# Kernel tuning notes

Hardware: AMD Instinct MI355X
Metric: run time of the kernel (lower is better)

The kernel has to match this reference:

```python
import jax, jax.numpy as jnp
import numpy as np

L_PAIRS = 2
K_NEG = 64
TEMP = 0.1
EPS = 1e-8  # torch F.cosine_similarity default eps


def _cos(a, b):
    # cosine similarity along last axis, torch-style eps clamping of norms
    na = jnp.maximum(jnp.linalg.norm(a, axis=-1), EPS)
    nb = jnp.maximum(jnp.linalg.norm(b, axis=-1), EPS)
    return jnp.sum(a * b, axis=-1) / (na * nb)


def setup_inputs() -> dict:
    D, N, d = 64, 4096, 512
    key = jax.random.key(0)
    k0, k1, k2, k3 = jax.random.split(key, 4)
    return {
        "I_embeddings": jax.random.normal(k0, (D, N, d), dtype=jnp.float32),
        "g0": jax.random.normal(k1, (d,), dtype=jnp.float32),
        "g1": jax.random.normal(k2, (d,), dtype=jnp.float32),
        "g2": jax.random.normal(k3, (d,), dtype=jnp.float32),
    }


def reference(I_embeddings, g0, g1, g2):
    D, N, d = I_embeddings.shape
    T = TEMP

    # per-embedding full sum: [D, d]
    sums = jnp.sum(I_embeddings, axis=1)

    # hard-negative sums: drop the top-K rows by L2 norm per embedding
    norms = jnp.linalg.norm(I_embeddings, axis=2)              # [D, N]
    _, topk_idx = jax.lax.top_k(norms, K_NEG)                  # [D, K]
    keep = jnp.ones((D, N), dtype=bool)
    keep = keep.at[jnp.arange(D)[:, None], topk_idx].set(False)
    sums_neg = jnp.sum(I_embeddings * keep[:, :, None], axis=1)  # [D, d]

    samples = jnp.concatenate([sums, sums_neg], axis=0)        # [2D, d]

    # positive pairs (i, i+L)
    P = D - L_PAIRS
    i_idx = jnp.arange(P)
    j_idx = i_idx + L_PAIRS

    # candidates per pair: arange(2D) with i and j removed (i < j)
    base = jnp.arange(2 * D - 2)                               # [2D-2]
    cand = base[None, :] + (base[None, :] >= i_idx[:, None]).astype(base.dtype)
    cand = cand + (cand >= j_idx[:, None]).astype(cand.dtype)  # [P, 2D-2]

    # random choice of K_NEG negatives per pair (deterministic key)
    key = jax.random.key(42)
    keys = jax.random.split(key, P)
    perm = jax.vmap(lambda k: jax.random.permutation(k, 2 * D - 2))(keys)[:, :K_NEG]
    sel = jnp.take_along_axis(cand, perm, axis=1)              # [P, K]
    negs = samples[sel]                                        # [P, K, d]

    pos_ij = _cos(g1, jax.lax.stop_gradient(g2)) / T           # scalar
    pos_ji = _cos(g2, jax.lax.stop_gradient(g1)) / T           # scalar

    s_i = sums[i_idx]                                          # [P, d]
    s_j = sums[j_idx]
    sim_i = _cos(s_i[:, None, :], negs) / T                    # [P, K]
    sim_j = _cos(s_j[:, None, :], negs) / T

    # -log( exp(pos) / (exp(pos) + sum exp(sim)) ) = logaddexp(pos, lse(sim)) - pos
    loss_i = jnp.logaddexp(pos_ij, jax.nn.logsumexp(sim_i, axis=1)) - pos_ij  # [P]
    loss_j = jnp.logaddexp(pos_ji, jax.nn.logsumexp(sim_j, axis=1)) - pos_ji

    return jnp.sum(loss_i + loss_j)
```

## Files before the change

### kernel.cpp

```cpp
#include <hip/hip_runtime.h>
#include <stdint.h>

#define D_EMB   64
#define N_ROWS  4096
#define DIM     512
#define KNEG    64
#define P_PAIRS 62
#define BPE     32
#define RPB     (N_ROWS / BPE)
#define NCHUNK  (D_EMB * BPE)
#define EPSN    1e-8f
#define INV_T   10.0f

__device__ __forceinline__ uint32_t rotl32(uint32_t v, uint32_t r) {
  return (v << r) | (v >> (32u - r));
}

__device__ __forceinline__ void threefry(uint32_t k0, uint32_t k1,
                                         uint32_t c0, uint32_t c1,
                                         uint32_t& o0, uint32_t& o1) {
  uint32_t ks0 = k0, ks1 = k1, ks2 = k0 ^ k1 ^ 0x1BD11BDAu;
  uint32_t x0 = c0 + ks0, x1 = c1 + ks1;
#define RG(a,b,c,d) \
  x0 += x1; x1 = rotl32(x1,a); x1 ^= x0; \
  x0 += x1; x1 = rotl32(x1,b); x1 ^= x0; \
  x0 += x1; x1 = rotl32(x1,c); x1 ^= x0; \
  x0 += x1; x1 = rotl32(x1,d); x1 ^= x0;
  RG(13,15,26,6)   x0 += ks1; x1 += ks2 + 1u;
  RG(17,29,16,24)  x0 += ks2; x1 += ks0 + 2u;
  RG(13,15,26,6)   x0 += ks0; x1 += ks1 + 3u;
  RG(17,29,16,24)  x0 += ks1; x1 += ks2 + 4u;
  RG(13,15,26,6)   x0 += ks2; x1 += ks0 + 5u;
#undef RG
  o0 = x0; o1 = x1;
}

__global__ __launch_bounds__(256, 8) void k_pass1(const float* __restrict__ I,
                                                  float* __restrict__ partial,
                                                  float* __restrict__ norms) {
  const int e = blockIdx.x >> 5, b = blockIdx.x & 31;
  const int t = threadIdx.x, lane = t & 63, w = t >> 6;
  const float4* base = reinterpret_cast<const float4*>(I) + (size_t)e * N_ROWS * (DIM / 4);
  const int nbase = b * RPB;
  __shared__ float lds[4 * DIM];
  __shared__ float nlds[RPB];
  float acc[8] = {0.f,0.f,0.f,0.f,0.f,0.f,0.f,0.f};

#define CONSUME(ii, Av, Bv)                                                   \
  {                                                                           \
    acc[0] += Av.x; acc[1] += Av.y; acc[2] += Av.z; acc[3] += Av.w;           \
    acc[4] += Bv.x; acc[5] += Bv.y; acc[6] += Bv.z; acc[7] += Bv.w;           \
    float sq = Av.x*Av.x + Av.y*Av.y + Av.z*Av.z + Av.w*Av.w                  \
             + Bv.x*Bv.x + Bv.y*Bv.y + Bv.z*Bv.z + Bv.w*Bv.w;                 \
    _Pragma("unroll")                                                         \
    for (int off = 32; off; off >>= 1) sq += __shfl_xor(sq, off);             \
    if (lane == 0) nlds[(ii) * 4 + w] = sqrtf(sq);                            \
  }

  const float4* r0 = base + (size_t)(nbase + w) * (DIM / 4);
  float4 A = r0[lane];
  float4 B = r0[lane + 64];
  for (int i = 0; i < RPB / 4 - 1; ++i) {
    const float4* rn = base + (size_t)(nbase + (i + 1) * 4 + w) * (DIM / 4);
    float4 An = rn[lane];
    float4 Bn = rn[lane + 64];
    CONSUME(i, A, B);
    A = An; B = Bn;
  }
  CONSUME(RPB / 4 - 1, A, B);
#undef CONSUME

  const int p0 = 4 * lane;
#pragma unroll
  for (int q = 0; q < 4; ++q) {
    lds[w * DIM + p0 + q]       = acc[q];
    lds[w * DIM + 256 + p0 + q] = acc[4 + q];
  }
  __syncthreads();
  float s0 = lds[t] + lds[DIM + t] + lds[2*DIM + t] + lds[3*DIM + t];
  float s1 = lds[256 + t] + lds[DIM + 256 + t] + lds[2*DIM + 256 + t] + lds[3*DIM + 256 + t];
  float* po = partial + (size_t)blockIdx.x * DIM;
  po[t] = s0;
  po[256 + t] = s1;
  if (t < RPB) norms[e * N_ROWS + nbase + t] = nlds[t];
}

__global__ __launch_bounds__(512) void k_embed(const float* __restrict__ I,
                                               const float* __restrict__ partial,
                                               const float* __restrict__ norms,
                                               const float* __restrict__ g1,
                                               const float* __restrict__ g2,
                                               float* __restrict__ samples,
                                               float* __restrict__ snorm,
                                               float* __restrict__ posp) {
  const int e = blockIdx.x;
  const int t = threadIdx.x, lane = t & 63, w = t >> 6;
  __shared__ float rA[8], rB[8], rC[8];

  if (e == D_EMB) {
    float x = g1[t], y = g2[t];
    float d = x * y, sa = x * x, sb = y * y;
#pragma unroll
    for (int off = 32; off; off >>= 1) {
      d  += __shfl_xor(d, off);
      sa += __shfl_xor(sa, off);
      sb += __shfl_xor(sb, off);
    }
    if (lane == 0) { rA[w] = d; rB[w] = sa; rC[w] = sb; }
    __syncthreads();
    if (t == 0) {
      float dt = 0.f, s1 = 0.f, s2 = 0.f;
      for (int q = 0; q < 8; ++q) { dt += rA[q]; s1 += rB[q]; s2 += rC[q]; }
      posp[0] = dt / (fmaxf(sqrtf(s1), EPSN) * fmaxf(sqrtf(s2), EPSN)) * INV_T;
    }
    return;
  }

  float v[8];
#pragma unroll
  for (int q = 0; q < 8; ++q) v[q] = norms[e * N_ROWS + q * DIM + t];
  float lmax = v[0]; int lidx = t;
#pragma unroll
  for (int q = 1; q < 8; ++q)
    if (v[q] > lmax) { lmax = v[q]; lidx = q * DIM + t; }

  __shared__ float wbv[8];
  __shared__ int   wbi[8];
  __shared__ int   topidx[KNEG];
  for (int k = 0; k < KNEG; ++k) {
    float bv = lmax; int bi = lidx;
#pragma unroll
    for (int off = 32; off; off >>= 1) {
      float ov = __shfl_xor(bv, off);
      int   oi = __shfl_xor(bi, off);
      if (ov > bv || (ov == bv && oi < bi)) { bv = ov; bi = oi; }
    }
    if (lane == 0) { wbv[w] = bv; wbi[w] = bi; }
    __syncthreads();
    float fv = wbv[0]; int fi = wbi[0];
#pragma unroll
    for (int q = 1; q < 8; ++q)
      if (wbv[q] > fv || (wbv[q] == fv && wbi[q] < fi)) { fv = wbv[q]; fi = wbi[q]; }
    if (t == (fi & (DIM - 1))) {
      v[fi >> 9] = -1e30f;
      lmax = v[0]; lidx = t;
#pragma unroll
      for (int q = 1; q < 8; ++q)
        if (v[q] > lmax) { lmax = v[q]; lidx = q * DIM + t; }
    }
    if (t == 0) topidx[k] = fi;
    __syncthreads();
  }

  float s = 0.f;
  for (int b2 = 0; b2 < BPE; ++b2)
    s += partial[(size_t)(e * BPE + b2) * DIM + t];

  const float* base = I + (size_t)e * N_ROWS * DIM;
  float a = 0.f;
#pragma unroll 4
  for (int k = 0; k < KNEG; ++k)
    a += base[(size_t)topidx[k] * DIM + t];
  float sn = s - a;

  float q1 = s * s, q2 = sn * sn;
#pragma unroll
  for (int off = 32; off; off >>= 1) {
    q1 += __shfl_xor(q1, off);
    q2 += __shfl_xor(q2, off);
  }
  if (lane == 0) { rA[w] = q1; rB[w] = q2; }
  __syncthreads();
  if (t == 0) {
    float n1 = 0.f, n2 = 0.f;
    for (int q = 0; q < 8; ++q) { n1 += rA[q]; n2 += rB[q]; }
    snorm[e]         = fmaxf(sqrtf(n1), EPSN);
    snorm[D_EMB + e] = fmaxf(sqrtf(n2), EPSN);
  }
  samples[(size_t)e * DIM + t]           = s;
  samples[(size_t)(D_EMB + e) * DIM + t] = sn;
}

__global__ __launch_bounds__(256) void k_p3p4(const float* __restrict__ samples,
                                              const float* __restrict__ snorm,
                                              const float* __restrict__ posp,
                                              float* __restrict__ pairloss,
                                              int* __restrict__ cnt2,
                                              float* __restrict__ out) {
  const int p = blockIdx.x;
  const int t = threadIdx.x, lane = t & 63, w = t >> 6;
  __shared__ uint32_t bits[126];
  __shared__ uint32_t sk[2];
  __shared__ int      sel[KNEG];
  __shared__ float    simi[KNEG], simj[KNEG];
  __shared__ int      flag;

  if (t == 0) {
    uint32_t kh, kl, a, b;
    threefry(0u, 42u, 0u, (uint32_t)p, kh, kl);
    threefry(kh, kl, 0u, 1u, a, b);
    sk[0] = a; sk[1] = b;
  }
  __syncthreads();
  if (t < 126) {
    uint32_t a, b;
    threefry(sk[0], sk[1], 0u, (uint32_t)t, a, b);
    bits[t] = a ^ b;
  }
  __syncthreads();
  if (t < 126) {
    const uint32_t myb = bits[t];
    int rank = 0;
    for (int j = 0; j < 126; ++j) {
      const uint32_t bj = bits[j];
      rank += ((bj < myb) || (bj == myb && j < t)) ? 1 : 0;
    }
    if (rank < KNEG) {
      int vv = t + (t >= p ? 1 : 0);
      vv += (vv >= p + 2 ? 1 : 0);
      sel[rank] = vv;
    }
  }
  __syncthreads();

  const float4* S = reinterpret_cast<const float4*>(samples);
  const float4 siA = S[p * 128 + lane],       siB = S[p * 128 + 64 + lane];
  const float4 sjA = S[(p + 2) * 128 + lane], sjB = S[(p + 2) * 128 + 64 + lane];
  const float ni = snorm[p], nj = snorm[p + 2];
  for (int k = w; k < KNEG; k += 4) {
    const int r = sel[k];
    const float4 vA = S[r * 128 + lane], vB = S[r * 128 + 64 + lane];
    float di = siA.x*vA.x + siA.y*vA.y + siA.z*vA.z + siA.w*vA.w
             + siB.x*vB.x + siB.y*vB.y + siB.z*vB.z + siB.w*vB.w;
    float dj = sjA.x*vA.x + sjA.y*vA.y + sjA.z*vA.z + sjA.w*vA.w
             + sjB.x*vB.x + sjB.y*vB.y + sjB.z*vB.z + sjB.w*vB.w;
#pragma unroll
    for (int off = 32; off; off >>= 1) {
      di += __shfl_xor(di, off);
      dj += __shfl_xor(dj, off);
    }
    if (lane == 0) {
      const float nr = snorm[r];
      simi[k] = di / (ni * nr) * INV_T;
      simj[k] = dj / (nj * nr) * INV_T;
    }
  }
  __syncthreads();
  if (t < KNEG) {
    const float xi = simi[t], xj = simj[t];
    float mi = xi, mj = xj;
#pragma unroll
    for (int off = 32; off; off >>= 1) {
      mi = fmaxf(mi, __shfl_xor(mi, off));
      mj = fmaxf(mj, __shfl_xor(mj, off));
    }
    float ei = expf(xi - mi), ej = expf(xj - mj);
#pragma unroll
    for (int off = 32; off; off >>= 1) {
      ei += __shfl_xor(ei, off);
      ej += __shfl_xor(ej, off);
    }
    if (t == 0) {
      const float pos = posp[0];
      const float lsei = mi + logf(ei), lsej = mj + logf(ej);
      const float li = fmaxf(pos, lsei) + log1pf(expf(-fabsf(pos - lsei))) - pos;
      const float lj = fmaxf(pos, lsej) + log1pf(expf(-fabsf(pos - lsej))) - pos;
      pairloss[p] = li + lj;
    }
  }
  __syncthreads();

  if (t == 0) {
    int old = __hip_atomic_fetch_add(cnt2, 1, __ATOMIC_ACQ_REL,
                                     __HIP_MEMORY_SCOPE_AGENT);
    flag = (old == P_PAIRS - 1) ? 1 : 0;
  }
  __syncthreads();
  const int trig = flag;
  __syncthreads();
  if (!trig) return;
  __builtin_amdgcn_fence(__ATOMIC_ACQUIRE, "agent");
  if (t < 64) {
    float vv = (t < P_PAIRS) ? pairloss[t] : 0.f;
#pragma unroll
    for (int off = 32; off; off >>= 1) vv += __shfl_xor(vv, off);
    if (t == 0) out[0] = vv;
  }
}

extern "C" void kernel_launch(void* const* d_in, const int* in_sizes, int n_in,
                              void* d_out, int out_size, void* d_ws, size_t ws_size,
                              hipStream_t stream) {
  const float* I  = (const float*)d_in[0];
  const float* g1 = (const float*)d_in[2];
  const float* g2 = (const float*)d_in[3];
  float* out = (float*)d_out;

  float* ws = (float*)d_ws;
  float* norms    = ws;
  float* partial  = ws + 262144;
  float* samples  = partial + 1048576;
  float* snorm    = samples + 65536;
  float* posp     = snorm + 128;
  float* pairloss = posp + 4;
  int*   cnt2     = (int*)(pairloss + 64);

  hipMemsetAsync(cnt2, 0, sizeof(int), stream);

  k_pass1<<<NCHUNK,    256, 0, stream>>>(I, partial, norms);
  k_embed<<<D_EMB + 1, 512, 0, stream>>>(I, partial, norms, g1, g2,
                                         samples, snorm, posp);
  k_p3p4 <<<P_PAIRS,   256, 0, stream>>>(samples, snorm, posp, pairloss,
                                         cnt2, out);
}
```

Before: 215.3 us.

## Replace block-synchronized top-K with per-wave sorted top-K merge

After: 190.4 us. 1.13x faster.

```diff
diff --git a/kernel.cpp b/kernel.cpp
--- a/kernel.cpp
+++ b/kernel.cpp
@@ -11,6 +11,7 @@
 #define NCHUNK  (D_EMB * BPE)
 #define EPSN    1e-8f
 #define INV_T   10.0f
+#define NEGINF  (-1e30f)
 
 __device__ __forceinline__ uint32_t rotl32(uint32_t v, uint32_t r) {
   return (v << r) | (v >> (32u - r));
@@ -41,35 +42,23 @@
   const int e = blockIdx.x >> 5, b = blockIdx.x & 31;
   const int t = threadIdx.x, lane = t & 63, w = t >> 6;
   const float4* base = reinterpret_cast<const float4*>(I) + (size_t)e * N_ROWS * (DIM / 4);
-  const int nbase = b * RPB;
+  float acc[8] = {0.f,0.f,0.f,0.f,0.f,0.f,0.f,0.f};
   __shared__ float lds[4 * DIM];
   __shared__ float nlds[RPB];
-  float acc[8] = {0.f,0.f,0.f,0.f,0.f,0.f,0.f,0.f};
-
-#define CONSUME(ii, Av, Bv)                                                   \
-  {                                                                           \
-    acc[0] += Av.x; acc[1] += Av.y; acc[2] += Av.z; acc[3] += Av.w;           \
-    acc[4] += Bv.x; acc[5] += Bv.y; acc[6] += Bv.z; acc[7] += Bv.w;           \
-    float sq = Av.x*Av.x + Av.y*Av.y + Av.z*Av.z + Av.w*Av.w                  \
-             + Bv.x*Bv.x + Bv.y*Bv.y + Bv.z*Bv.z + Bv.w*Bv.w;                 \
-    _Pragma("unroll")                                                         \
-    for (int off = 32; off; off >>= 1) sq += __shfl_xor(sq, off);             \
-    if (lane == 0) nlds[(ii) * 4 + w] = sqrtf(sq);                            \
-  }
-
-  const float4* r0 = base + (size_t)(nbase + w) * (DIM / 4);
-  float4 A = r0[lane];
-  float4 B = r0[lane + 64];
-  for (int i = 0; i < RPB / 4 - 1; ++i) {
-    const float4* rn = base + (size_t)(nbase + (i + 1) * 4 + w) * (DIM / 4);
-    float4 An = rn[lane];
-    float4 Bn = rn[lane + 64];
-    CONSUME(i, A, B);
-    A = An; B = Bn;
-  }
-  CONSUME(RPB / 4 - 1, A, B);
-#undef CONSUME
-
+  const int nbase = b * RPB;
+  for (int i = 0; i < RPB / 4; ++i) {
+    const int n = nbase + i * 4 + w;
+    const float4* row = base + (size_t)n * (DIM / 4);
+    float4 A = row[lane];
+    float4 B = row[lane + 64];
+    acc[0] += A.x; acc[1] += A.y; acc[2] += A.z; acc[3] += A.w;
+    acc[4] += B.x; acc[5] += B.y; acc[6] += B.z; acc[7] += B.w;
+    float sq = A.x*A.x + A.y*A.y + A.z*A.z + A.w*A.w
+             + B.x*B.x + B.y*B.y + B.z*B.z + B.w*B.w;
+#pragma unroll
+    for (int off = 32; off; off >>= 1) sq += __shfl_xor(sq, off);
+    if (lane == 0) nlds[i * 4 + w] = sqrtf(sq);
+  }
   const int p0 = 4 * lane;
 #pragma unroll
   for (int q = 0; q < 4; ++q) {
@@ -84,6 +73,12 @@
   po[256 + t] = s1;
   if (t < RPB) norms[e * N_ROWS + nbase + t] = nlds[t];
 }
+
+#define CE(i, j) \
+  { bool sw = (v##i < v##j) || (v##i == v##j && d##i > d##j);          \
+    float tv = sw ? v##j : v##i; float uv = sw ? v##i : v##j;          \
+    int   td = sw ? d##j : d##i; int   ud = sw ? d##i : d##j;          \
+    v##i = tv; v##j = uv; d##i = td; d##j = ud; }
 
 __global__ __launch_bounds__(512) void k_embed(const float* __restrict__ I,
                                                const float* __restrict__ partial,
@@ -92,12 +87,14 @@
                                                const float* __restrict__ g2,
                                                float* __restrict__ samples,
                                                float* __restrict__ snorm,
-                                               float* __restrict__ posp) {
+                                               float* __restrict__ posp,
+                                               int* __restrict__ cnt2) {
   const int e = blockIdx.x;
   const int t = threadIdx.x, lane = t & 63, w = t >> 6;
   __shared__ float rA[8], rB[8], rC[8];
 
   if (e == D_EMB) {
+    if (t == 0) cnt2[0] = 0;
     float x = g1[t], y = g2[t];
     float d = x * y, sa = x * x, sb = y * y;
 #pragma unroll
@@ -116,41 +113,60 @@
     return;
   }
 
-  float v[8];
-#pragma unroll
-  for (int q = 0; q < 8; ++q) v[q] = norms[e * N_ROWS + q * DIM + t];
-  float lmax = v[0]; int lidx = t;
-#pragma unroll
-  for (int q = 1; q < 8; ++q)
-    if (v[q] > lmax) { lmax = v[q]; lidx = q * DIM + t; }
-
-  __shared__ float wbv[8];
-  __shared__ int   wbi[8];
+  __shared__ float cval[8 * KNEG];
+  __shared__ int   cidx[8 * KNEG];
   __shared__ int   topidx[KNEG];
+
+  float v0 = norms[e*N_ROWS + 0*512 + t], v1 = norms[e*N_ROWS + 1*512 + t];
+  float v2 = norms[e*N_ROWS + 2*512 + t], v3 = norms[e*N_ROWS + 3*512 + t];
+  float v4 = norms[e*N_ROWS + 4*512 + t], v5 = norms[e*N_ROWS + 5*512 + t];
+  float v6 = norms[e*N_ROWS + 6*512 + t], v7 = norms[e*N_ROWS + 7*512 + t];
+  int d0 = 0*512+t, d1 = 1*512+t, d2 = 2*512+t, d3 = 3*512+t;
+  int d4 = 4*512+t, d5 = 5*512+t, d6 = 6*512+t, d7 = 7*512+t;
+  CE(0,1) CE(2,3) CE(4,5) CE(6,7)
+  CE(0,2) CE(1,3) CE(4,6) CE(5,7)
+  CE(1,2) CE(5,6)
+  CE(0,4) CE(1,5) CE(2,6) CE(3,7)
+  CE(2,4) CE(3,5)
+  CE(1,2) CE(3,4) CE(5,6)
+
   for (int k = 0; k < KNEG; ++k) {
-    float bv = lmax; int bi = lidx;
+    float bv = v0; int bi = d0;
 #pragma unroll
     for (int off = 32; off; off >>= 1) {
       float ov = __shfl_xor(bv, off);
       int   oi = __shfl_xor(bi, off);
       if (ov > bv || (ov == bv && oi < bi)) { bv = ov; bi = oi; }
     }
-    if (lane == 0) { wbv[w] = bv; wbi[w] = bi; }
-    __syncthreads();
-    float fv = wbv[0]; int fi = wbi[0];
-#pragma unroll
-    for (int q = 1; q < 8; ++q)
-      if (wbv[q] > fv || (wbv[q] == fv && wbi[q] < fi)) { fv = wbv[q]; fi = wbi[q]; }
-    if (t == (fi & (DIM - 1))) {
-      v[fi >> 9] = -1e30f;
-      lmax = v[0]; lidx = t;
-#pragma unroll
-      for (int q = 1; q < 8; ++q)
-        if (v[q] > lmax) { lmax = v[q]; lidx = q * DIM + t; }
-    }
-    if (t == 0) topidx[k] = fi;
-    __syncthreads();
-  }
+    if (lane == 0) { cval[w * KNEG + k] = bv; cidx[w * KNEG + k] = bi; }
+    if (v0 == bv && d0 == bi) {
+      v0=v1; d0=d1; v1=v2; d1=d2; v2=v3; d2=d3; v3=v4; d3=d4;
+      v4=v5; d4=d5; v5=v6; d5=d6; v6=v7; d6=d7; v7=NEGINF; d7=0x7fffffff;
+    }
+  }
+  __syncthreads();
+
+  if (w == 0) {
+    int p = 0;
+    float hv = (lane < 8) ? cval[lane * KNEG] : NEGINF;
+    int   hi = (lane < 8) ? cidx[lane * KNEG] : 0x7fffffff;
+    for (int k = 0; k < KNEG; ++k) {
+      float bv = hv; int bi = hi;
+#pragma unroll
+      for (int off = 4; off; off >>= 1) {
+        float ov = __shfl_xor(bv, off, 8);
+        int   oi = __shfl_xor(bi, off, 8);
+        if (ov > bv || (ov == bv && oi < bi)) { bv = ov; bi = oi; }
+      }
+      if (lane == 0) topidx[k] = bi;
+      if (lane < 8 && hv == bv && hi == bi) {
+        ++p;
+        hv = (p < KNEG) ? cval[lane * KNEG + p] : NEGINF;
+        hi = (p < KNEG) ? cidx[lane * KNEG + p] : 0x7fffffff;
+      }
+    }
+  }
+  __syncthreads();
 
   float s = 0.f;
   for (int b2 = 0; b2 < BPE; ++b2)
@@ -305,11 +321,9 @@
   float* pairloss = posp + 4;
   int*   cnt2     = (int*)(pairloss + 64);
 
-  hipMemsetAsync(cnt2, 0, sizeof(int), stream);
-
   k_pass1<<<NCHUNK,    256, 0, stream>>>(I, partial, norms);
   k_embed<<<D_EMB + 1, 512, 0, stream>>>(I, partial, norms, g1, g2,
-                                         samples, snorm, posp);
+                                         samples, snorm, posp, cnt2);
   k_p3p4 <<<P_PAIRS,   256, 0, stream>>>(samples, snorm, posp, pairloss,
                                          cnt2, out);
 }
```
